# Kernel tuning notes

Hardware: AMD Instinct MI355X
Metric: run time of the kernel (lower is better)

## Reference

```python
import jax, jax.numpy as jnp
import numpy as np

N = 1024      # nodes
E = 16384     # edges
Q = 8192      # query pairs
H1 = 32       # hidden_dim_1
H2 = 32       # hidden_dim_2
MAXX = 100    # max node label
EPS = 1e-5


def setup_inputs() -> dict:
    key = jax.random.key(0)
    ks = jax.random.split(key, 16)
    nrm = lambda k, shp, s=0.05: jax.random.normal(k, shp, jnp.float32) * s
    inp = {
        "x_ids": jax.random.randint(ks[0], (N,), 0, MAXX + 1),
        "ei": jax.random.randint(ks[1], (2, E), 0, N),
        "pos": jax.random.randint(ks[2], (Q, 2), 0, N),
        # embedding table
        "emb": nrm(ks[3], (MAXX + 1, H1)),
        # GCN layer 0 (lin + bias) and GraphNorm 0 (gamma, beta, mean-scale alpha)
        "gcn_w0": nrm(ks[4], (H1, H1)), "gcn_b0": jnp.zeros((H1,), jnp.float32),
        "gn0_g": jnp.ones((H1,), jnp.float32), "gn0_b": jnp.zeros((H1,), jnp.float32), "gn0_a": jnp.ones((H1,), jnp.float32),
        # GCN layer 1 + GraphNorm 1
        "gcn_w1": nrm(ks[5], (H1, H1)), "gcn_b1": jnp.zeros((H1,), jnp.float32),
        "gn1_g": jnp.ones((H1,), jnp.float32), "gn1_b": jnp.zeros((H1,), jnp.float32), "gn1_a": jnp.ones((H1,), jnp.float32),
        # mlps_1 / mlps_2: Linear(H1+1 -> H2)
        "w_m1": nrm(ks[6], (H1 + 1, H2)), "b_m1": jnp.zeros((H2,), jnp.float32),
        "w_m2": nrm(ks[7], (H1 + 1, H2)), "b_m2": jnp.zeros((H2,), jnp.float32),
        # mlps_3: Linear(H2 + H1 + 1 -> H2) + GraphNorm
        "w_m3": nrm(ks[8], (H2 + H1 + 1, H2)), "b_m3": jnp.zeros((H2,), jnp.float32),
        "gn3_g": jnp.ones((H2,), jnp.float32), "gn3_b": jnp.zeros((H2,), jnp.float32), "gn3_a": jnp.ones((H2,), jnp.float32),
        # lin_dir: Linear(H2 -> 1)
        "w_dir": nrm(ks[9], (H2, 1)), "b_dir": jnp.zeros((1,), jnp.float32),
    }
    return inp


def _graphnorm(x, g, b, a):
    # GraphNorm: per-feature norm over all node (leading) dims, learnable mean-scale a
    ax = tuple(range(x.ndim - 1))
    mu = jnp.mean(x, axis=ax, keepdims=True)
    xc = x - a * mu
    var = jnp.mean(xc * xc, axis=ax, keepdims=True)
    return g * xc * jax.lax.rsqrt(var + EPS) + b


def _gcn(x, src, dst, W, b, n):
    # PyG GCNConv: sym-normalized aggregation with added self-loops
    deg = jnp.zeros((n,), x.dtype).at[dst].add(1.0) + 1.0  # +1 self loop
    dinv = jax.lax.rsqrt(deg)
    h = x @ W
    coef = dinv[src] * dinv[dst]                 # [E]
    agg = jnp.zeros_like(h).at[dst].add(h[src] * coef[:, None])
    agg = agg + h * (dinv * dinv)[:, None]       # self-loop term
    return agg + b


def _forward(x_ids, ei, pos, emb,
             gcn_w0, gcn_b0, gn0_g, gn0_b, gn0_a,
             gcn_w1, gcn_b1, gn1_g, gn1_b, gn1_a,
             w_m1, b_m1, w_m2, b_m2, w_m3, b_m3, gn3_g, gn3_b, gn3_a,
             w_dir, b_dir):
    n = x_ids.shape[0]
    src, dst = ei[0], ei[1]
    x = emb[x_ids]                                        # [n, H1]
    # layer1 = 2 GCN blocks: GCNConv -> GraphNorm -> (Dropout p=0) -> ReLU
    x = jax.nn.relu(_graphnorm(_gcn(x, src, dst, gcn_w0, gcn_b0, n), gn0_g, gn0_b, gn0_a))
    x = jax.nn.relu(_graphnorm(_gcn(x, src, dst, gcn_w1, gcn_b1, n), gn1_g, gn1_b, gn1_a))
    # pairwise 2-tensor: rowx * colx -> [n, n, H1]
    pair = x[:, None, :] * x[None, :, :]
    # adjacency indicator; eye @ eim == eim (single matrix-power step)
    eim = jnp.zeros((n, n), x.dtype).at[src, dst].set(1.0)
    x = jnp.concatenate([pair, eim[:, :, None]], axis=-1)  # [n, n, H1+1]
    # layer2 = 1 FWL block
    x1 = jax.nn.relu(x @ w_m1 + b_m1)                      # [n, n, H2]
    x2 = jax.nn.relu(x @ w_m2 + b_m2)                      # [n, n, H2]
    prod = jnp.einsum('ijc,jkc->ikc', x1, x2)              # per-channel n x n matmul
    x = jnp.concatenate([x, prod], axis=-1)                # [n, n, H1+1+H2]
    x = jax.nn.relu(_graphnorm(x @ w_m3 + b_m3, gn3_g, gn3_b, gn3_a))
    # mul_pool: symmetric multiply then gather query pairs
    x = (x * jnp.transpose(x, (1, 0, 2))).reshape(n * n, -1)
    x = x[pos[:, 0] * n + pos[:, 1]]                       # [Q, H2]
    return x @ w_dir + b_dir                               # [Q, 1]


def reference(x_ids, ei, pos, emb,
              gcn_w0, gcn_b0, gn0_g, gn0_b, gn0_a,
              gcn_w1, gcn_b1, gn1_g, gn1_b, gn1_a,
              w_m1, b_m1, w_m2, b_m2, w_m3, b_m3, gn3_g, gn3_b, gn3_a,
              w_dir, b_dir):
    return _forward(x_ids, ei, pos, emb,
                    gcn_w0, gcn_b0, gn0_g, gn0_b, gn0_a,
                    gcn_w1, gcn_b1, gn1_g, gn1_b, gn1_a,
                    w_m1, b_m1, w_m2, b_m2, w_m3, b_m3, gn3_g, gn3_b, gn3_a,
                    w_dir, b_dir)
```

## Files before the change

### kernel.cpp

```cpp
#include <hip/hip_runtime.h>
#include <hip/hip_bf16.h>
#include <cstddef>

constexpr int   kN  = 1024;
constexpr int   kE  = 16384;
constexpr int   kQ  = 8192;
constexpr int   kH  = 32;
constexpr size_t kNN = (size_t)kN * kN;
constexpr float kEPS = 1e-5f;
constexpr int   kCWg = 8;
constexpr int   kCWb = 16;
constexpr int   kStatsBlocks = kN;

using short8 = __attribute__((ext_vector_type(8))) short;
using f32x4  = __attribute__((ext_vector_type(4))) float;

__device__ __forceinline__ unsigned short f2bf(float f) {
    __hip_bfloat16 h = __float2bfloat16(f);
    return *reinterpret_cast<unsigned short*>(&h);
}


__global__ void k_edge(const int* __restrict__ ei, float* __restrict__ deg,
                       unsigned char* __restrict__ adj, unsigned char* __restrict__ adjT) {
    int e = blockIdx.x * 256 + threadIdx.x;
    if (e < kE) {
        int s = ei[e], d = ei[kE + e];
        atomicAdd(&deg[d], 1.0f);
        adj [s * kN + d] = 1;
        adjT[d * kN + s] = 1;
    }
}

__global__ void k_dinv(const float* __restrict__ deg, float* __restrict__ dinv) {
    int n = blockIdx.x * 256 + threadIdx.x;
    if (n < kN) dinv[n] = rsqrtf(deg[n] + 1.0f);
}

__global__ void k_embed(const int* __restrict__ xids, const float* __restrict__ emb,
                        float* __restrict__ x0) {
    int t = blockIdx.x * 256 + threadIdx.x;
    int n = t >> 5, c = t & 31;
    x0[t] = emb[xids[n] * kH + c];
}

__global__ void k_node_mm(const float* __restrict__ x, const float* __restrict__ W,
                          float* __restrict__ h) {
    __shared__ float Ws[kH * kH];
    int t = threadIdx.x;
    for (int u = t; u < kH * kH; u += 256) Ws[u] = W[u];
    __syncthreads();
    int g = blockIdx.x * 256 + t;
    int n = g >> 5, c = g & 31;
    float acc = 0.f;
#pragma unroll
    for (int d = 0; d < kH; d++) acc = fmaf(x[n * kH + d], Ws[d * kH + c], acc);
    h[g] = acc;
}

__global__ void k_scatter(const int* __restrict__ ei, const float* __restrict__ h,
                          const float* __restrict__ dinv, float* __restrict__ agg) {
    int t = blockIdx.x * 256 + threadIdx.x;
    int e = t >> 5, c = t & 31;
    int s = ei[e], d = ei[kE + e];
    atomicAdd(&agg[d * kH + c], h[s * kH + c] * dinv[s] * dinv[d]);
}

__global__ void k_gcn_post(float* __restrict__ agg, const float* __restrict__ h,
                           const float* __restrict__ dinv, const float* __restrict__ b) {
    int t = blockIdx.x * 256 + threadIdx.x;
    int n = t >> 5, c = t & 31;
    agg[t] += h[t] * dinv[n] * dinv[n] + b[c];
}

__global__ void k_graphnorm(const float* __restrict__ x, float* __restrict__ out,
                            const float* __restrict__ g, const float* __restrict__ b,
                            const float* __restrict__ a, int M) {
    int c = blockIdx.x, t = threadIdx.x;
    float s = 0.f, ss = 0.f;
    for (int m = t; m < M; m += 256) { float v = x[m * kH + c]; s += v; ss += v * v; }
    __shared__ float rs[256], rss[256];
    rs[t] = s; rss[t] = ss;
    __syncthreads();
    for (int o = 128; o > 0; o >>= 1) {
        if (t < o) { rs[t] += rs[t + o]; rss[t] += rss[t + o]; }
        __syncthreads();
    }
    __shared__ float scale, shift;
    if (t == 0) {
        float mu  = rs[0] / (float)M;
        float ac  = a[c];
        float var = rss[0] / (float)M - 2.f * ac * mu * mu + ac * ac * mu * mu;
        float sc  = g[c] * rsqrtf(var + kEPS);
        scale = sc;
        shift = b[c] - sc * ac * mu;
    }
    __syncthreads();
    for (int m = t; m < M; m += 256) {
        float v = scale * x[m * kH + c] + shift;
        out[m * kH + c] = v > 0.f ? v : 0.f;
    }
}


template<int CW>
__global__ __launch_bounds__(256) void k_genxz(
        const float* __restrict__ xn,
        const unsigned char* __restrict__ adj, const unsigned char* __restrict__ adjT,
        const float* __restrict__ w1, const float* __restrict__ b1,
        const float* __restrict__ w2, const float* __restrict__ b2,
        __hip_bfloat16* __restrict__ X1, __hip_bfloat16* __restrict__ X2t, int c0base) {
    static_assert(CW * 32 == 256, "store re-partition assumes CW*32 == blockDim");
    int zc = blockIdx.z;
    int c0 = c0base + (zc >> 1) * CW;
    const unsigned char* adjX = (zc & 1) ? adjT : adj;
    const float* w = (zc & 1) ? w2 : w1;
    const float* b = (zc & 1) ? b2 : b1;
    __hip_bfloat16* X = ((zc & 1) ? X2t : X1) + (size_t)(zc >> 1) * CW * kNN;
    int o = blockIdx.y;
    int t = threadIdx.x;
    int i0 = blockIdx.x * 256;
    int in = i0 + t;

    __shared__ float xis[256][kH + 1];
    for (int u = t; u < 256 * kH; u += 256)
        xis[u >> 5][u & 31] = xn[(size_t)i0 * kH + u];
    __syncthreads();

    float p[kH];
#pragma unroll
    for (int d = 0; d < kH; d++)
        p[d] = xn[o * kH + d] * xis[t][d];
    float e = (float)adjX[o * kN + in];
    float v[CW];
#pragma unroll
    for (int cc = 0; cc < CW; cc++) v[cc] = b[c0 + cc];
#pragma unroll
    for (int d = 0; d < kH; d++) {
#pragma unroll
        for (int cc = 0; cc < CW; cc++)
            v[cc] = fmaf(p[d], w[d * kH + c0 + cc], v[cc]);
    }
    __shared__ unsigned short lds[CW][256];
    __syncthreads();
#pragma unroll
    for (int cc = 0; cc < CW; cc++) {
        float r = fmaf(e, w[32 * kH + c0 + cc], v[cc]);
        lds[cc][t] = f2bf(r > 0.f ? r : 0.f);
    }
    __syncthreads();
    int cc = t >> 5, seg = t & 31;
    short8 val = *(const short8*)&lds[cc][seg * 8];
    unsigned short* Xp = (unsigned short*)X;
    *(short8*)&Xp[(size_t)cc * kNN + (size_t)o * kN + i0 + seg * 8] = val;
}


__device__ __forceinline__ void g2l16(const unsigned short* g, unsigned short* l) {
    __builtin_amdgcn_global_load_lds(
        (const __attribute__((address_space(1))) void*)g,
        (__attribute__((address_space(3))) void*)l, 16, 0, 0);
}

__global__ __launch_bounds__(256) void k_bgemm_bf16(
        const unsigned short* __restrict__ A_, const unsigned short* __restrict__ Bt_,
        float* __restrict__ C_) {
    int b = blockIdx.x + 8 * blockIdx.y + 64 * blockIdx.z;
    int g = b & 7;
    int r = b >> 3;
    int c = 2 * g + (r >> 6);
    int tile = r & 63;
    int j0 = (tile & 7) * 128;
    int i0 = (tile >> 3) * 128;
    const unsigned short* A  = A_  + (size_t)c * kNN;
    const unsigned short* Bt = Bt_ + (size_t)c * kNN;
    float* C = C_ + (size_t)c * kNN;
    __shared__ unsigned short As[128 * 64];
    __shared__ unsigned short Bs[128 * 64];
    int t = threadIdx.x;
    int lane = t & 63, w = t >> 6;
    int wr = (w >> 1) * 64, wc = (w & 1) * 64;
    int l15 = lane & 15, lhi = lane >> 4;
    int srow = t >> 3, skel = (t & 7) * 8;
    f32x4 acc[4][4] = {};
    for (int k0 = 0; k0 < kN; k0 += 64) {
#pragma unroll
        for (int qq = 0; qq < 4; qq++) {
            g2l16(A  + (size_t)(i0 + srow + qq * 32) * kN + k0 + skel,
                  As + ((size_t)t + qq * 256) * 8);
            g2l16(Bt + (size_t)(j0 + srow + qq * 32) * kN + k0 + skel,
                  Bs + ((size_t)t + qq * 256) * 8);
        }
        asm volatile("s_waitcnt vmcnt(0)" ::: "memory");
        __syncthreads();
#pragma unroll
        for (int ks = 0; ks < 2; ks++) {
            short8 af[4], bf[4];
#pragma unroll
            for (int m = 0; m < 4; m++)
                af[m] = *(const short8*)&As[(wr + m * 16 + l15) * 64 + ks * 32 + lhi * 8];
#pragma unroll
            for (int n = 0; n < 4; n++)
                bf[n] = *(const short8*)&Bs[(wc + n * 16 + l15) * 64 + ks * 32 + lhi * 8];
#pragma unroll
            for (int m = 0; m < 4; m++)
#pragma unroll
                for (int n = 0; n < 4; n++)
                    acc[m][n] = __builtin_amdgcn_mfma_f32_16x16x32_bf16(af[m], bf[n], acc[m][n], 0, 0, 0);
        }
        __syncthreads();
    }
#pragma unroll
    for (int m = 0; m < 4; m++) {
        int row = i0 + wr + m * 16 + lhi * 4;
#pragma unroll
        for (int n = 0; n < 4; n++) {
            int col = j0 + wc + n * 16 + l15;
#pragma unroll
            for (int r2 = 0; r2 < 4; r2++)
                C[(size_t)(row + r2) * kN + col] = acc[m][n][r2];
        }
    }
}


__global__ __launch_bounds__(256) void k_stats_mfma(
        const float* __restrict__ xn, const unsigned char* __restrict__ adj,
        const float* __restrict__ prod, const float* __restrict__ w3,
        const float* __restrict__ b3, float* __restrict__ spart) {
    __shared__ unsigned short As[128 * 104];
    __shared__ unsigned short Bs[32 * 104];
    __shared__ float xi[kH], lsum[kH], lssq[kH];
    int t = threadIdx.x;
    int i = blockIdx.x;
    int lane = t & 63, w = t >> 6;
    int l15 = lane & 15, lhi = lane >> 4;

    for (int u = t; u < 128 * 104 / 8; u += 256)
        *(short8*)&As[u * 8] = short8{0, 0, 0, 0, 0, 0, 0, 0};
    {
        int c = t & 31, s0 = (t >> 5) * 13;
        for (int s = s0; s < s0 + 13; s++) {
            float v = 0.f;
            if (s <= 32)                 v = w3[s * kH + c];
            else if (s >= 34 && s <= 65) v = w3[(s - 1) * kH + c];
            else if (s == 66)            v = b3[c];
            Bs[c * 104 + s] = f2bf(v);
        }
    }
    if (t < kH) { xi[t] = xn[i * kH + t]; lsum[t] = 0.f; lssq[t] = 0.f; }
    __syncthreads();
    if (t < 128) As[t * 104 + 66] = f2bf(1.0f);

    float s2[2] = {0.f, 0.f}, q22[2] = {0.f, 0.f};
    int wrow = w * 32;

    for (int kt = 0; kt < 8; kt++) {
        int kbase = kt * 128;
        {
            int r = t >> 1, half = t & 1;
            int k = kbase + r;
            const float* xr = &xn[k * kH + half * 16];
            float4 v0 = *(const float4*)&xr[0];
            float4 v1 = *(const float4*)&xr[4];
            float4 v2 = *(const float4*)&xr[8];
            float4 v3 = *(const float4*)&xr[12];
            const float* xih = &xi[half * 16];
            short8 o0, o1;
            o0[0] = f2bf(xih[0] * v0.x);  o0[1] = f2bf(xih[1] * v0.y);
            o0[2] = f2bf(xih[2] * v0.z);  o0[3] = f2bf(xih[3] * v0.w);
            o0[4] = f2bf(xih[4] * v1.x);  o0[5] = f2bf(xih[5] * v1.y);
            o0[6] = f2bf(xih[6] * v1.z);  o0[7] = f2bf(xih[7] * v1.w);
            o1[0] = f2bf(xih[8] * v2.x);  o1[1] = f2bf(xih[9] * v2.y);
            o1[2] = f2bf(xih[10] * v2.z); o1[3] = f2bf(xih[11] * v2.w);
            o1[4] = f2bf(xih[12] * v3.x); o1[5] = f2bf(xih[13] * v3.y);
            o1[6] = f2bf(xih[14] * v3.z); o1[7] = f2bf(xih[15] * v3.w);
            *(short8*)&As[r * 104 + half * 16]     = o0;
            *(short8*)&As[r * 104 + half * 16 + 8] = o1;
        }
        if (t < 128) As[t * 104 + 32] = f2bf((float)adj[i * kN + kbase + t]);
        {
            int kq = t & 15, dp = t >> 4, d2 = dp * 2;
            const float* p0 = &prod[(size_t)d2 * kNN + (size_t)i * kN + kbase + kq * 8];
            const float* p1 = p0 + kNN;
            float4 a0 = *(const float4*)&p0[0];
            float4 a1 = *(const float4*)&p0[4];
            float4 b0 = *(const float4*)&p1[0];
            float4 b1 = *(const float4*)&p1[4];
            float r0[8] = {a0.x, a0.y, a0.z, a0.w, a1.x, a1.y, a1.z, a1.w};
            float r1[8] = {b0.x, b0.y, b0.z, b0.w, b1.x, b1.y, b1.z, b1.w};
            unsigned int* As32 = (unsigned int*)As;
#pragma unroll
            for (int j = 0; j < 8; j++) {
                int jr = (j + kq) & 7;
                int kl = kq * 8 + jr;
                unsigned int val = (unsigned int)f2bf(r0[jr]) |
                                   ((unsigned int)f2bf(r1[jr]) << 16);
                As32[kl * 52 + 17 + dp] = val;
            }
        }
        __syncthreads();
        f32x4 acc[2][2] = {};
#pragma unroll
        for (int ks = 0; ks < 3; ks++) {
            short8 af0 = *(const short8*)&As[(wrow + l15) * 104 + ks * 32 + lhi * 8];
            short8 af1 = *(const short8*)&As[(wrow + 16 + l15) * 104 + ks * 32 + lhi * 8];
            short8 bf0 = *(const short8*)&Bs[l15 * 104 + ks * 32 + lhi * 8];
            short8 bf1 = *(const short8*)&Bs[(16 + l15) * 104 + ks * 32 + lhi * 8];
            acc[0][0] = __builtin_amdgcn_mfma_f32_16x16x32_bf16(af0, bf0, acc[0][0], 0, 0, 0);
            acc[0][1] = __builtin_amdgcn_mfma_f32_16x16x32_bf16(af0, bf1, acc[0][1], 0, 0, 0);
            acc[1][0] = __builtin_amdgcn_mfma_f32_16x16x32_bf16(af1, bf0, acc[1][0], 0, 0, 0);
            acc[1][1] = __builtin_amdgcn_mfma_f32_16x16x32_bf16(af1, bf1, acc[1][1], 0, 0, 0);
        }
#pragma unroll
        for (int ct = 0; ct < 2; ct++)
#pragma unroll
            for (int rt = 0; rt < 2; rt++)
#pragma unroll
                for (int r = 0; r < 4; r++) {
                    float y = acc[rt][ct][r];
                    s2[ct] += y;
                    q22[ct] = fmaf(y, y, q22[ct]);
                }
        __syncthreads();
    }
#pragma unroll
    for (int ct = 0; ct < 2; ct++) {
        s2[ct]  += __shfl_xor(s2[ct], 16);  s2[ct]  += __shfl_xor(s2[ct], 32);
        q22[ct] += __shfl_xor(q22[ct], 16); q22[ct] += __shfl_xor(q22[ct], 32);
    }
    if (lane < 16) {
#pragma unroll
        for (int ct = 0; ct < 2; ct++) {
            atomicAdd(&lsum[ct * 16 + l15], s2[ct]);
            atomicAdd(&lssq[ct * 16 + l15], q22[ct]);
        }
    }
    __syncthreads();
    if (t < kH)          spart[(size_t)i * 64 + t]             = lsum[t];
    else if (t < 2 * kH) spart[(size_t)i * 64 + 32 + (t - kH)] = lssq[t - kH];
}

__global__ __launch_bounds__(256) void k_reduce(const float* __restrict__ spart,
                                                float* __restrict__ stats) {
    int slot = blockIdx.x;
    int t = threadIdx.x;
    float acc = 0.f;
    for (int r = t; r < kStatsBlocks; r += 256) acc += spart[(size_t)r * 64 + slot];
    __shared__ float red[256];
    red[t] = acc;
    __syncthreads();
    for (int o = 128; o > 0; o >>= 1) {
        if (t < o) red[t] += red[t + o];
        __syncthreads();
    }
    if (t == 0) stats[slot] = red[0];
}

__global__ void k_finalize(const float* __restrict__ stats, const float* __restrict__ g,
                           const float* __restrict__ b, const float* __restrict__ a,
                           float* __restrict__ ss) {
    int c = threadIdx.x;
    float M   = (float)((double)kNN);
    float mu  = stats[c] / M;
    float ac  = a[c];
    float var = stats[kH + c] / M - 2.f * ac * mu * mu + ac * ac * mu * mu;
    float sc  = g[c] * rsqrtf(var + kEPS);
    ss[c]      = sc;
    ss[kH + c] = b[c] - sc * ac * mu;
}


__global__ __launch_bounds__(256) void k_out(
        const int* __restrict__ pos, const float* __restrict__ xn,
        const unsigned char* __restrict__ adj, const float* __restrict__ prod,
        const float* __restrict__ w3, const float* __restrict__ b3,
        const float* __restrict__ ss, const float* __restrict__ wdir,
        const float* __restrict__ bdir, float* __restrict__ out) {
    __shared__ float W3s[65 * kH], b3s[kH], scs[kH], shs[kH], wd[kH];
    int t = threadIdx.x;
    for (int u = t; u < 65 * kH; u += 256) W3s[u] = w3[u];
    if (t < kH) { b3s[t] = b3[t]; scs[t] = ss[t]; shs[t] = ss[kH + t]; wd[t] = wdir[t]; }
    __syncthreads();
    int q = blockIdx.x * 4 + (t >> 6);
    int lane = t & 63;
    int c = lane & 31, h = lane >> 5;
    int i = pos[2 * q], k = pos[2 * q + 1];
    size_t addr = h ? ((size_t)k * kN + i) : ((size_t)i * kN + k);
    float pr_reg = prod[(size_t)c * kNN + addr];
    float p_reg  = xn[i * kH + c] * xn[k * kH + c];
    float e_reg  = (float)adj[addr];
    float y = b3s[c];
#pragma unroll
    for (int d = 0; d < kH; d++)
        y = fmaf(__shfl(p_reg, d), W3s[d * kH + c], y);
    y = fmaf(e_reg, W3s[32 * kH + c], y);
#pragma unroll
    for (int d = 0; d < kH; d++)
        y = fmaf(__shfl(pr_reg, (h << 5) + d), W3s[(33 + d) * kH + c], y);
    float z = scs[c] * y + shs[c];
    z = z > 0.f ? z : 0.f;
    float zo = __shfl_xor(z, 32);
    float v = z * zo * wd[c];
#pragma unroll
    for (int o = 16; o > 0; o >>= 1) v += __shfl_xor(v, o);
    if (lane == 0) out[q] = v + bdir[0];
}


extern "C" void kernel_launch(void* const* d_in, const int* in_sizes, int n_in,
                              void* d_out, int out_size, void* d_ws, size_t ws_size,
                              hipStream_t stream) {
    const int*   x_ids = (const int*)d_in[0];
    const int*   ei    = (const int*)d_in[1];
    const int*   pos   = (const int*)d_in[2];
    const float* emb   = (const float*)d_in[3];
    const float* gw0   = (const float*)d_in[4];
    const float* gb0   = (const float*)d_in[5];
    const float* g0g   = (const float*)d_in[6];
    const float* g0b   = (const float*)d_in[7];
    const float* g0a   = (const float*)d_in[8];
    const float* gw1   = (const float*)d_in[9];
    const float* gb1   = (const float*)d_in[10];
    const float* g1g   = (const float*)d_in[11];
    const float* g1b   = (const float*)d_in[12];
    const float* g1a   = (const float*)d_in[13];
    const float* wm1   = (const float*)d_in[14];
    const float* bm1   = (const float*)d_in[15];
    const float* wm2   = (const float*)d_in[16];
    const float* bm2   = (const float*)d_in[17];
    const float* wm3   = (const float*)d_in[18];
    const float* bm3   = (const float*)d_in[19];
    const float* g3g   = (const float*)d_in[20];
    const float* g3b   = (const float*)d_in[21];
    const float* g3a   = (const float*)d_in[22];
    const float* wdir  = (const float*)d_in[23];
    const float* bdir  = (const float*)d_in[24];
    float* out = (float*)d_out;

    const size_t fixedF = (size_t)kH * kNN;
    float* prod = (float*)d_ws;
    unsigned short* X1c = (unsigned short*)(prod + fixedF);
    unsigned short* X2c = X1c + (size_t)kCWb * kNN;
    unsigned char* adj  = (unsigned char*)(X2c + (size_t)kCWb * kNN);
    unsigned char* adjT = adj + kNN;
    float* deg   = (float*)(adjT + kNN);
    float* dinv  = deg + kN;
    float* x0    = dinv + kN;
    float* h     = x0 + kN * kH;
    float* agg   = h + kN * kH;
    float* xa    = agg + kN * kH;
    float* xb    = xa + kN * kH;
    float* spart = xb + kN * kH;
    float* stats = spart + (size_t)kStatsBlocks * 64;
    float* ss    = stats + 2 * kH;

    hipMemsetAsync(deg, 0, kN * sizeof(float), stream);
    hipMemsetAsync(adj, 0, 2 * kNN, stream);
    hipMemsetAsync(agg, 0, kN * kH * sizeof(float), stream);

    k_edge<<<(kE + 255) / 256, 256, 0, stream>>>(ei, deg, adj, adjT);
    k_dinv<<<4, 256, 0, stream>>>(deg, dinv);
    k_embed<<<kN * kH / 256, 256, 0, stream>>>(x_ids, emb, x0);

    k_node_mm<<<kN * kH / 256, 256, 0, stream>>>(x0, gw0, h);
    k_scatter<<<kE * kH / 256, 256, 0, stream>>>(ei, h, dinv, agg);
    k_gcn_post<<<kN * kH / 256, 256, 0, stream>>>(agg, h, dinv, gb0);
    k_graphnorm<<<kH, 256, 0, stream>>>(agg, xa, g0g, g0b, g0a, kN);

    hipMemsetAsync(agg, 0, kN * kH * sizeof(float), stream);
    k_node_mm<<<kN * kH / 256, 256, 0, stream>>>(xa, gw1, h);
    k_scatter<<<kE * kH / 256, 256, 0, stream>>>(ei, h, dinv, agg);
    k_gcn_post<<<kN * kH / 256, 256, 0, stream>>>(agg, h, dinv, gb1);
    k_graphnorm<<<kH, 256, 0, stream>>>(agg, xb, g1g, g1b, g1a, kN);

    for (int c0 = 0; c0 < kH; c0 += kCWb) {
        k_genxz<kCWg><<<dim3(4, kN, 4), 256, 0, stream>>>(
            xb, adj, adjT, wm1, bm1, wm2, bm2,
            (__hip_bfloat16*)X1c, (__hip_bfloat16*)X2c, c0);
        k_bgemm_bf16<<<dim3(8, 8, kCWb), 256, 0, stream>>>(X1c, X2c, prod + (size_t)c0 * kNN);
    }

    k_stats_mfma<<<kStatsBlocks, 256, 0, stream>>>(xb, adj, prod, wm3, bm3, spart);
    k_reduce<<<64, 256, 0, stream>>>(spart, stats);
    k_finalize<<<1, 32, 0, stream>>>(stats, g3g, g3b, g3a, ss);

    k_out<<<kQ / 4, 256, 0, stream>>>(pos, xb, adj, prod, wm3, bm3, ss, wdir, bdir, out);
}
```

Before: 413.0 us.

## Generate FWL x1/x2 pair features with bf16 MFMA instead of scalar FMA

```diff
diff --git a/kernel.cpp b/kernel.cpp
--- a/kernel.cpp
+++ b/kernel.cpp
@@ -8,7 +8,6 @@
 constexpr int   kH  = 32;
 constexpr size_t kNN = (size_t)kN * kN;
 constexpr float kEPS = 1e-5f;
-constexpr int   kCWg = 8;
 constexpr int   kCWb = 16;
 constexpr int   kStatsBlocks = kN;
 
@@ -18,6 +17,9 @@
 __device__ __forceinline__ unsigned short f2bf(float f) {
     __hip_bfloat16 h = __float2bfloat16(f);
     return *reinterpret_cast<unsigned short*>(&h);
+}
+__device__ __forceinline__ unsigned int packbf2(float a, float b) {
+    return (unsigned int)f2bf(a) | ((unsigned int)f2bf(b) << 16);
 }
 
 
@@ -103,56 +105,102 @@
 }
 
 
-template<int CW>
-__global__ __launch_bounds__(256) void k_genxz(
+__global__ __launch_bounds__(256) void k_genx_mfma(
         const float* __restrict__ xn,
         const unsigned char* __restrict__ adj, const unsigned char* __restrict__ adjT,
         const float* __restrict__ w1, const float* __restrict__ b1,
         const float* __restrict__ w2, const float* __restrict__ b2,
-        __hip_bfloat16* __restrict__ X1, __hip_bfloat16* __restrict__ X2t, int c0base) {
-    static_assert(CW * 32 == 256, "store re-partition assumes CW*32 == blockDim");
-    int zc = blockIdx.z;
-    int c0 = c0base + (zc >> 1) * CW;
-    const unsigned char* adjX = (zc & 1) ? adjT : adj;
-    const float* w = (zc & 1) ? w2 : w1;
-    const float* b = (zc & 1) ? b2 : b1;
-    __hip_bfloat16* X = ((zc & 1) ? X2t : X1) + (size_t)(zc >> 1) * CW * kNN;
-    int o = blockIdx.y;
+        unsigned short* __restrict__ X1, unsigned short* __restrict__ X2t, int c0) {
+    __shared__ unsigned short As[128 * 72];
+    __shared__ unsigned short Bs[32 * 72];
+    __shared__ unsigned short outb[32 * 136];
     int t = threadIdx.x;
-    int i0 = blockIdx.x * 256;
-    int in = i0 + t;
-
-    __shared__ float xis[256][kH + 1];
-    for (int u = t; u < 256 * kH; u += 256)
-        xis[u >> 5][u & 31] = xn[(size_t)i0 * kH + u];
-    __syncthreads();
-
-    float p[kH];
-#pragma unroll
-    for (int d = 0; d < kH; d++)
-        p[d] = xn[o * kH + d] * xis[t][d];
-    float e = (float)adjX[o * kN + in];
-    float v[CW];
-#pragma unroll
-    for (int cc = 0; cc < CW; cc++) v[cc] = b[c0 + cc];
-#pragma unroll
-    for (int d = 0; d < kH; d++) {
-#pragma unroll
-        for (int cc = 0; cc < CW; cc++)
-            v[cc] = fmaf(p[d], w[d * kH + c0 + cc], v[cc]);
-    }
-    __shared__ unsigned short lds[CW][256];
-    __syncthreads();
-#pragma unroll
-    for (int cc = 0; cc < CW; cc++) {
-        float r = fmaf(e, w[32 * kH + c0 + cc], v[cc]);
-        lds[cc][t] = f2bf(r > 0.f ? r : 0.f);
-    }
-    __syncthreads();
-    int cc = t >> 5, seg = t & 31;
-    short8 val = *(const short8*)&lds[cc][seg * 8];
-    unsigned short* Xp = (unsigned short*)X;
-    *(short8*)&Xp[(size_t)cc * kNN + (size_t)o * kN + i0 + seg * 8] = val;
+    int in0 = blockIdx.x * 128;
+    int o   = blockIdx.y;
+    int lane = t & 63, w = t >> 6;
+    int l15 = lane & 15, lhi = lane >> 4;
+
+    for (int u = t; u < 1152; u += 256) *(short8*)&As[u * 8] = short8{0,0,0,0,0,0,0,0};
+    for (int u = t; u < 288; u += 256)  *(short8*)&Bs[u * 8] = short8{0,0,0,0,0,0,0,0};
+    __syncthreads();
+
+    {
+        int row = t >> 1, half = t & 1;
+        int in = in0 + row;
+        const float* xr = &xn[(size_t)in * kH + half * 16];
+        float4 v0 = *(const float4*)&xr[0];
+        float4 v1 = *(const float4*)&xr[4];
+        float4 v2 = *(const float4*)&xr[8];
+        float4 v3 = *(const float4*)&xr[12];
+        const float* xo = &xn[(size_t)o * kH + half * 16];
+        short8 o0, o1;
+        o0[0] = f2bf(xo[0] * v0.x);  o0[1] = f2bf(xo[1] * v0.y);
+        o0[2] = f2bf(xo[2] * v0.z);  o0[3] = f2bf(xo[3] * v0.w);
+        o0[4] = f2bf(xo[4] * v1.x);  o0[5] = f2bf(xo[5] * v1.y);
+        o0[6] = f2bf(xo[6] * v1.z);  o0[7] = f2bf(xo[7] * v1.w);
+        o1[0] = f2bf(xo[8] * v2.x);  o1[1] = f2bf(xo[9] * v2.y);
+        o1[2] = f2bf(xo[10] * v2.z); o1[3] = f2bf(xo[11] * v2.w);
+        o1[4] = f2bf(xo[12] * v3.x); o1[5] = f2bf(xo[13] * v3.y);
+        o1[6] = f2bf(xo[14] * v3.z); o1[7] = f2bf(xo[15] * v3.w);
+        *(short8*)&As[row * 72 + half * 16]     = o0;
+        *(short8*)&As[row * 72 + half * 16 + 8] = o1;
+    }
+    if (t < 128) {
+        As[t * 72 + 32] = f2bf((float)adj [o * kN + in0 + t]);
+        As[t * 72 + 33] = f2bf((float)adjT[o * kN + in0 + t]);
+        As[t * 72 + 34] = f2bf(1.0f);
+    }
+    if (t < 32) {
+        int n = t;
+        int ch = c0 + (n & 15);
+        const float* wsel = (n < 16) ? w1 : w2;
+        const float* bsel = (n < 16) ? b1 : b2;
+        for (int d = 0; d < kH; d++) Bs[n * 72 + d] = f2bf(wsel[d * kH + ch]);
+        Bs[n * 72 + 32] = (n < 16) ? f2bf(w1[32 * kH + ch]) : (unsigned short)0;
+        Bs[n * 72 + 33] = (n < 16) ? (unsigned short)0 : f2bf(w2[32 * kH + ch]);
+        Bs[n * 72 + 34] = f2bf(bsel[ch]);
+    }
+    __syncthreads();
+
+    int wrow = w * 32;
+    f32x4 acc[2][2] = {};
+#pragma unroll
+    for (int ks = 0; ks < 2; ks++) {
+        short8 af0 = *(const short8*)&As[(wrow + l15) * 72 + ks * 32 + lhi * 8];
+        short8 af1 = *(const short8*)&As[(wrow + 16 + l15) * 72 + ks * 32 + lhi * 8];
+        short8 bf0 = *(const short8*)&Bs[l15 * 72 + ks * 32 + lhi * 8];
+        short8 bf1 = *(const short8*)&Bs[(16 + l15) * 72 + ks * 32 + lhi * 8];
+        acc[0][0] = __builtin_amdgcn_mfma_f32_16x16x32_bf16(af0, bf0, acc[0][0], 0, 0, 0);
+        acc[0][1] = __builtin_amdgcn_mfma_f32_16x16x32_bf16(af0, bf1, acc[0][1], 0, 0, 0);
+        acc[1][0] = __builtin_amdgcn_mfma_f32_16x16x32_bf16(af1, bf0, acc[1][0], 0, 0, 0);
+        acc[1][1] = __builtin_amdgcn_mfma_f32_16x16x32_bf16(af1, bf1, acc[1][1], 0, 0, 0);
+    }
+    unsigned int* ob32 = (unsigned int*)outb;
+#pragma unroll
+    for (int mi = 0; mi < 2; mi++) {
+        int brow = wrow + mi * 16 + lhi * 4;
+#pragma unroll
+        for (int nt = 0; nt < 2; nt++) {
+            int ch = nt * 16 + l15;
+            float y0 = acc[mi][nt][0]; y0 = y0 > 0.f ? y0 : 0.f;
+            float y1 = acc[mi][nt][1]; y1 = y1 > 0.f ? y1 : 0.f;
+            float y2 = acc[mi][nt][2]; y2 = y2 > 0.f ? y2 : 0.f;
+            float y3 = acc[mi][nt][3]; y3 = y3 > 0.f ? y3 : 0.f;
+            ob32[ch * 68 + (brow >> 1)]     = packbf2(y0, y1);
+            ob32[ch * 68 + (brow >> 1) + 1] = packbf2(y2, y3);
+        }
+    }
+    __syncthreads();
+    {
+        int ch = t >> 3, seg = t & 7;
+        short8 v0 = *(const short8*)&outb[ch * 136 + seg * 16];
+        short8 v1 = *(const short8*)&outb[ch * 136 + seg * 16 + 8];
+        unsigned short* base = (ch < 16) ? (X1 + (size_t)ch * kNN)
+                                         : (X2t + (size_t)(ch - 16) * kNN);
+        size_t off = (size_t)o * kN + in0 + seg * 16;
+        *(short8*)&base[off]     = v0;
+        *(short8*)&base[off + 8] = v1;
+    }
 }
 
 
@@ -475,9 +523,8 @@
     k_graphnorm<<<kH, 256, 0, stream>>>(agg, xb, g1g, g1b, g1a, kN);
 
     for (int c0 = 0; c0 < kH; c0 += kCWb) {
-        k_genxz<kCWg><<<dim3(4, kN, 4), 256, 0, stream>>>(
-            xb, adj, adjT, wm1, bm1, wm2, bm2,
-            (__hip_bfloat16*)X1c, (__hip_bfloat16*)X2c, c0);
+        k_genx_mfma<<<dim3(8, kN), 256, 0, stream>>>(
+            xb, adj, adjT, wm1, bm1, wm2, bm2, X1c, X2c, c0);
         k_bgemm_bf16<<<dim3(8, 8, kCWb), 256, 0, stream>>>(X1c, X2c, prod + (size_t)c0 * kNN);
     }
 
```

Measured after the change: 371.0 us. -10.2%, faster.
